# Optimization experiments

Measured on AMD Instinct MI355X. Metric: run time of the kernel, lower is better.

The kernel has to match this reference:

```python
import jax, jax.numpy as jnp
import numpy as np

D_MODEL = 1024
D_STATE = 512
SEQ_LEN = 16384
R_MIN, R_MAX, MAX_PHASE = 0.0, 1.0, 6.28


def setup_inputs() -> dict:
    key = jax.random.key(0)
    ks = jax.random.split(key, 8)
    inputs = jax.random.normal(ks[0], (SEQ_LEN, D_MODEL), dtype=jnp.float32)
    # parameter init exactly as in the module
    u_nu = jax.random.uniform(ks[1], (D_STATE,), dtype=jnp.float32)
    nu_log = jnp.log(-0.5 * jnp.log(u_nu * (R_MAX ** 2 - R_MIN ** 2) + R_MIN ** 2))
    u_th = jax.random.uniform(ks[2], (D_STATE,), dtype=jnp.float32)
    theta_log = jnp.log(MAX_PHASE * u_th)
    diag_lambda = jnp.exp(-jnp.exp(nu_log) + 1j * jnp.exp(theta_log))
    gamma_log = jnp.log(jnp.sqrt(1.0 - jnp.abs(diag_lambda) ** 2))
    bn = jnp.sqrt(jnp.asarray(2 * D_MODEL, jnp.float32))
    cn = jnp.sqrt(jnp.asarray(D_STATE, jnp.float32))
    B_re = jax.random.normal(ks[3], (D_STATE, D_MODEL), dtype=jnp.float32) / bn
    B_im = jax.random.normal(ks[4], (D_STATE, D_MODEL), dtype=jnp.float32) / bn
    C_re = jax.random.normal(ks[5], (D_MODEL, D_STATE), dtype=jnp.float32) / cn
    C_im = jax.random.normal(ks[6], (D_MODEL, D_STATE), dtype=jnp.float32) / cn
    D = jax.random.normal(ks[7], (D_MODEL,), dtype=jnp.float32)
    return {"inputs": inputs, "nu_log": nu_log, "theta_log": theta_log,
            "gamma_log": gamma_log, "B_re": B_re, "B_im": B_im,
            "C_re": C_re, "C_im": C_im, "D": D}


def _binop(q_i, q_j):
    # associative combine for diagonal linear recurrence h' = a*h + b
    a_i, b_i = q_i
    a_j, b_j = q_j
    return (a_j * a_i, a_j * b_i + b_j)


def reference(inputs, nu_log, theta_log, gamma_log, B_re, B_im, C_re, C_im, D):
    L = inputs.shape[0]
    diag_lambda = jnp.exp(-jnp.exp(nu_log) + 1j * jnp.exp(theta_log))  # (d_state,)
    B_norm = (B_re + 1j * B_im) * jnp.exp(gamma_log)[:, None]          # (d_state, d_model)
    C = C_re + 1j * C_im                                               # (d_model, d_state)
    # Bu[t] = B_norm @ x_t  -> (L, d_state) complex
    Bu = inputs.astype(B_norm.dtype) @ B_norm.T
    Lambda_elems = jnp.broadcast_to(diag_lambda, (L, diag_lambda.shape[0]))
    _, h = jax.lax.associative_scan(_binop, (Lambda_elems, Bu))        # (L, d_state)
    # y_t = Re[C h_t] + D * x_t
    return jnp.real(h @ C.T) + D * inputs
```

## Files before the change

### kernel.cpp

```cpp
#include <hip/hip_runtime.h>
#include <math.h>

#define L_SEQ   16384
#define DMODEL  1024
#define NST     512
#define CHUNK   128
#define NCHUNK  (L_SEQ / CHUNK)

typedef float  f32x4 __attribute__((ext_vector_type(4)));
typedef short  s16x8 __attribute__((ext_vector_type(8)));

__device__ __forceinline__ unsigned short f2bf(float f) {
    union { float f; unsigned int u; } v; v.f = f;
    unsigned int r = v.u + 0x7fffu + ((v.u >> 16) & 1u);
    return (unsigned short)(r >> 16);
}
__device__ __forceinline__ unsigned short f2bf_fast(float f) {
    union { float f; unsigned int u; } v; v.f = f;
    return (unsigned short)((v.u + 0x8000u) >> 16);
}
__device__ __forceinline__ float bf2f(unsigned int h16) {
    union { unsigned int u; float f; } v; v.u = h16 << 16; return v.f;
}
__device__ __forceinline__ void mfma16(f32x4& d, s16x8 a, s16x8 b) {
    asm volatile("v_mfma_f32_16x16x32_bf16 %0, %1, %2, %0"
                 : "+v"(d) : "v"(a), "v"(b));
}
__device__ __forceinline__ uint4 pack8(float4 x, float4 y) {
    union { unsigned short u[8]; uint4 v; } t;
    t.u[0] = f2bf_fast(x.x); t.u[1] = f2bf_fast(x.y);
    t.u[2] = f2bf_fast(x.z); t.u[3] = f2bf_fast(x.w);
    t.u[4] = f2bf_fast(y.x); t.u[5] = f2bf_fast(y.y);
    t.u[6] = f2bf_fast(y.z); t.u[7] = f2bf_fast(y.w);
    return t.v;
}

__global__ void setup_params(const float* __restrict__ nu_log,
                             const float* __restrict__ theta_log,
                             float* __restrict__ lam,
                             float* __restrict__ lamH,
                             float* __restrict__ lamT) {
    int s = threadIdx.x;
    if (s >= NST) return;
    float mod = expf(-expf(nu_log[s]));
    float th  = expf(theta_log[s]);
    float ar = mod * cosf(th);
    float ai = mod * sinf(th);
    lam[s] = ar; lam[NST + s] = ai;
    float pr = 1.f, pi = 0.f;
    for (int i = 0; i < CHUNK; ++i) {
        float nr = pr * ar - pi * ai;
        float ni = pr * ai + pi * ar;
        pr = nr; pi = ni;
        if (i == 63) { lamH[s] = pr; lamH[NST + s] = pi; }
    }
    lamT[s] = pr; lamT[NST + s] = pi;
}

__global__ void pack_w1(const float* __restrict__ Bre, const float* __restrict__ Bim,
                        const float* __restrict__ gamma_log, unsigned short* __restrict__ W1) {
    int idx = blockIdx.x * 256 + threadIdx.x;
    int n = idx >> 10, k = idx & 1023;
    int s = n >> 1;
    float g = expf(gamma_log[s]);
    float v = (n & 1) ? Bim[s * DMODEL + k] : Bre[s * DMODEL + k];
    W1[idx] = f2bf(v * g);
}
__global__ void pack_w2(const float* __restrict__ Cre, const float* __restrict__ Cim,
                        unsigned short* __restrict__ W2) {
    int idx = blockIdx.x * 256 + threadIdx.x;
    int n = idx >> 10, k = idx & 1023;
    int s = k >> 1;
    float v = (k & 1) ? -Cim[n * NST + s] : Cre[n * NST + s];
    W2[idx] = f2bf(v);
}

__global__ __launch_bounds__(256)
void gemm1_scan(const float* __restrict__ X, const unsigned short* __restrict__ W1,
                const float* __restrict__ lam,
                unsigned int* __restrict__ Bu, float* __restrict__ ends) {
    const int K = 1024;
    __shared__ __align__(16) unsigned short As[128 * 32];
    __shared__ __align__(16) unsigned short Bs[128 * 32];
    __shared__ __align__(16) unsigned short Ts[128 * 132];

    const int tid  = threadIdx.x;
    const int lane = tid & 63;
    const int wave = tid >> 6;
    const int wr   = wave >> 1, wc = wave & 1;

    const int lin   = blockIdx.y * gridDim.x + blockIdx.x;
    const int n_new = (lin & 7) * 128 + (lin >> 3);
    const int bx = n_new & 7, by = n_new >> 3;
    const int m0 = by * 128, n0 = bx * 128;

    const int srow = tid >> 2;
    const int skb  = (tid & 3) * 8;

    const float*          Ag0 = X  + (size_t)(m0 + srow) * K + skb;
    const float*          Ag1 = Ag0 + (size_t)64 * K;
    const unsigned short* Bg0 = W1 + (size_t)(n0 + srow) * K + skb;
    const unsigned short* Bg1 = Bg0 + (size_t)64 * K;

    f32x4 acc[4][4] = {};

    float4 a00 = *(const float4*)(Ag0);
    float4 a01 = *(const float4*)(Ag0 + 4);
    float4 a10 = *(const float4*)(Ag1);
    float4 a11 = *(const float4*)(Ag1 + 4);
    uint4  rb0 = *(const uint4*)(Bg0);
    uint4  rb1 = *(const uint4*)(Bg1);

    const int fr = lane & 15;
    const int fk = (lane >> 4) * 8;

    for (int k0 = 0; k0 < K; k0 += 32) {
        __syncthreads();
        *(uint4*)&As[srow * 32 + skb]        = pack8(a00, a01);
        *(uint4*)&As[(64 + srow) * 32 + skb] = pack8(a10, a11);
        *(uint4*)&Bs[srow * 32 + skb]        = rb0;
        *(uint4*)&Bs[(64 + srow) * 32 + skb] = rb1;
        __syncthreads();
        if (k0 + 32 < K) {
            a00 = *(const float4*)(Ag0 + k0 + 32);
            a01 = *(const float4*)(Ag0 + k0 + 36);
            a10 = *(const float4*)(Ag1 + k0 + 32);
            a11 = *(const float4*)(Ag1 + k0 + 36);
            rb0 = *(const uint4*)(Bg0 + k0 + 32);
            rb1 = *(const uint4*)(Bg1 + k0 + 32);
        }
        s16x8 af[4], bfq[4];
        #pragma unroll
        for (int i = 0; i < 4; ++i)
            af[i] = *(const s16x8*)&As[(wr * 64 + i * 16 + fr) * 32 + fk];
        #pragma unroll
        for (int j = 0; j < 4; ++j)
            bfq[j] = *(const s16x8*)&Bs[(wc * 64 + j * 16 + fr) * 32 + fk];
        #pragma unroll
        for (int i = 0; i < 4; ++i)
            #pragma unroll
            for (int j = 0; j < 4; ++j)
                mfma16(acc[i][j], af[i], bfq[j]);
    }

    const int crow = (lane >> 4) * 4;
    const int ccol = lane & 15;
    #pragma unroll
    for (int i = 0; i < 4; ++i)
        #pragma unroll
        for (int j = 0; j < 4; ++j)
            #pragma unroll
            for (int r = 0; r < 4; ++r)
                Ts[(wr * 64 + i * 16 + crow + r) * 132 + wc * 64 + j * 16 + ccol]
                    = f2bf_fast(acc[i][j][r]);
    __syncthreads();

    if (tid < 64) {
        const int s  = (n0 >> 1) + tid;
        const float lr = lam[s], li = lam[NST + s];
        float hr = 0.f, hi = 0.f;
        size_t gb = (size_t)m0 * NST + s;
        for (int t = 0; t < 128; ++t) {
            unsigned int v = *(const unsigned int*)&Ts[t * 132 + 2 * tid];
            float br = bf2f(v & 0xffffu), bi = bf2f(v >> 16);
            float nr = fmaf(lr, hr, fmaf(-li, hi, br));
            float ni = fmaf(lr, hi, fmaf( li, hr, bi));
            hr = nr; hi = ni;
            Bu[gb + (size_t)t * NST] =
                (unsigned int)f2bf_fast(hr) | ((unsigned int)f2bf_fast(hi) << 16);
        }
        ends[(size_t)(by * NST + s) * 2]     = hr;
        ends[(size_t)(by * NST + s) * 2 + 1] = hi;
    }
}

__global__ __launch_bounds__(NST)
void scan_carry(const float* __restrict__ ends, const float* __restrict__ lamT,
                float* __restrict__ car) {
    const int s = threadIdx.x;
    const float ar = lamT[s], ai = lamT[NST + s];
    float cr = 0.f, ci = 0.f;
    for (int c = 0; c < NCHUNK; ++c) {
        car[(size_t)(c * NST + s) * 2]     = cr;
        car[(size_t)(c * NST + s) * 2 + 1] = ci;
        float er = ends[(size_t)(c * NST + s) * 2];
        float ei = ends[(size_t)(c * NST + s) * 2 + 1];
        float nr = fmaf(ar, cr, fmaf(-ai, ci, er));
        float ni = fmaf(ar, ci, fmaf( ai, cr, ei));
        cr = nr; ci = ni;
    }
}

__global__ __launch_bounds__(NST)
void scan_apply(unsigned int* __restrict__ Bu, const float* __restrict__ lam,
                const float* __restrict__ lamH, const float* __restrict__ car) {
    const int c    = blockIdx.x >> 1;
    const int half = blockIdx.x & 1;
    if (c == 0) return;
    const int s = threadIdx.x;
    const float lr = lam[s], li = lam[NST + s];
    float pr = car[(size_t)(c * NST + s) * 2];
    float pi = car[(size_t)(c * NST + s) * 2 + 1];
    if (half) {
        float hr = lamH[s], hi = lamH[NST + s];
        float nr = pr * hr - pi * hi;
        float ni = pr * hi + pi * hr;
        pr = nr; pi = ni;
    }
    size_t base = ((size_t)c * CHUNK + half * 64) * NST + s;
    #pragma unroll 4
    for (int t = 0; t < 64; ++t) {
        float nr = lr * pr - li * pi;
        float ni = lr * pi + li * pr;
        pr = nr; pi = ni;
        unsigned int v = Bu[base + (size_t)t * NST];
        float hr = bf2f(v & 0xffffu) + pr;
        float hi = bf2f(v >> 16)     + pi;
        Bu[base + (size_t)t * NST] =
            (unsigned int)f2bf_fast(hr) | ((unsigned int)f2bf_fast(hi) << 16);
    }
}

__global__ __launch_bounds__(256)
void gemm2(const unsigned short* __restrict__ H, const unsigned short* __restrict__ W2,
           float* __restrict__ Y, const float* __restrict__ Dv,
           const float* __restrict__ Xf) {
    const int K = 1024, N = 1024;
    __shared__ __align__(16) unsigned short As[128 * 32];
    __shared__ __align__(16) unsigned short Bs[128 * 32];

    const int tid  = threadIdx.x;
    const int lane = tid & 63;
    const int wave = tid >> 6;
    const int wr   = wave >> 1, wc = wave & 1;

    const int lin   = blockIdx.y * gridDim.x + blockIdx.x;
    const int n_new = (lin & 7) * 128 + (lin >> 3);
    const int bx = n_new & 7, by = n_new >> 3;
    const int m0 = by * 128, n0 = bx * 128;

    const int srow = tid >> 2;
    const int skb  = (tid & 3) * 8;

    const unsigned short* Ag0 = H  + (size_t)(m0 + srow) * K + skb;
    const unsigned short* Ag1 = Ag0 + (size_t)64 * K;
    const unsigned short* Bg0 = W2 + (size_t)(n0 + srow) * K + skb;
    const unsigned short* Bg1 = Bg0 + (size_t)64 * K;

    f32x4 acc[4][4] = {};

    uint4 ra0 = *(const uint4*)Ag0;
    uint4 ra1 = *(const uint4*)Ag1;
    uint4 rb0 = *(const uint4*)Bg0;
    uint4 rb1 = *(const uint4*)Bg1;

    const int fr = lane & 15;
    const int fk = (lane >> 4) * 8;

    for (int k0 = 0; k0 < K; k0 += 32) {
        __syncthreads();
        *(uint4*)&As[srow * 32 + skb]        = ra0;
        *(uint4*)&As[(64 + srow) * 32 + skb] = ra1;
        *(uint4*)&Bs[srow * 32 + skb]        = rb0;
        *(uint4*)&Bs[(64 + srow) * 32 + skb] = rb1;
        __syncthreads();
        if (k0 + 32 < K) {
            ra0 = *(const uint4*)(Ag0 + k0 + 32);
            ra1 = *(const uint4*)(Ag1 + k0 + 32);
            rb0 = *(const uint4*)(Bg0 + k0 + 32);
            rb1 = *(const uint4*)(Bg1 + k0 + 32);
        }
        s16x8 af[4], bfq[4];
        #pragma unroll
        for (int i = 0; i < 4; ++i)
            af[i] = *(const s16x8*)&As[(wr * 64 + i * 16 + fr) * 32 + fk];
        #pragma unroll
        for (int j = 0; j < 4; ++j)
            bfq[j] = *(const s16x8*)&Bs[(wc * 64 + j * 16 + fr) * 32 + fk];
        #pragma unroll
        for (int i = 0; i < 4; ++i)
            #pragma unroll
            for (int j = 0; j < 4; ++j)
                mfma16(acc[i][j], af[i], bfq[j]);
    }

    const int crow = (lane >> 4) * 4;
    const int ccol = lane & 15;
    #pragma unroll
    for (int i = 0; i < 4; ++i) {
        #pragma unroll
        for (int j = 0; j < 4; ++j) {
            const int mbase = m0 + wr * 64 + i * 16 + crow;
            const int n     = n0 + wc * 64 + j * 16 + ccol;
            #pragma unroll
            for (int r = 0; r < 4; ++r) {
                const int m = mbase + r;
                Y[(size_t)m * N + n] = acc[i][j][r] + Dv[n] * Xf[(size_t)m * N + n];
            }
        }
    }
}

extern "C" void kernel_launch(void* const* d_in, const int* in_sizes, int n_in,
                              void* d_out, int out_size, void* d_ws, size_t ws_size,
                              hipStream_t stream) {
    const float* X         = (const float*)d_in[0];
    const float* nu_log    = (const float*)d_in[1];
    const float* theta_log = (const float*)d_in[2];
    const float* gamma_log = (const float*)d_in[3];
    const float* Bre       = (const float*)d_in[4];
    const float* Bim       = (const float*)d_in[5];
    const float* Cre       = (const float*)d_in[6];
    const float* Cim       = (const float*)d_in[7];
    const float* Dv        = (const float*)d_in[8];
    float* Y = (float*)d_out;

    char* ws = (char*)d_ws;
    size_t off = 0;
    unsigned int*   Bu  = (unsigned int*)(ws + off);   off += (size_t)L_SEQ * NST * 4;
    unsigned short* W1  = (unsigned short*)(ws + off); off += (size_t)DMODEL * DMODEL * 2;
    unsigned short* W2  = (unsigned short*)(ws + off); off += (size_t)DMODEL * DMODEL * 2;
    float* lam  = (float*)(ws + off); off += 1024 * 4;
    float* lamH = (float*)(ws + off); off += 1024 * 4;
    float* lamT = (float*)(ws + off); off += 1024 * 4;
    float* ends = (float*)(ws + off); off += (size_t)NCHUNK * NST * 2 * 4;
    float* car  = (float*)(ws + off); off += (size_t)NCHUNK * NST * 2 * 4;

    setup_params<<<1, NST, 0, stream>>>(nu_log, theta_log, lam, lamH, lamT);
    pack_w1<<<(DMODEL * DMODEL) / 256, 256, 0, stream>>>(Bre, Bim, gamma_log, W1);
    pack_w2<<<(DMODEL * DMODEL) / 256, 256, 0, stream>>>(Cre, Cim, W2);

    dim3 gg(8, 128);
    gemm1_scan<<<gg, 256, 0, stream>>>(X, W1, lam, Bu, ends);
    scan_carry<<<1, NST, 0, stream>>>(ends, lamT, car);
    scan_apply<<<2 * NCHUNK, NST, 0, stream>>>(Bu, lam, lamH, car);
    gemm2<<<gg, 256, 0, stream>>>((const unsigned short*)Bu, W2, Y, Dv, X);
}
```

Baseline: 156.4 us.

## Split fused GEMM+chunk scan into separate GEMM, chunk-end scan and full rescan

The chunk-local scan that ran inside the GEMM1 epilogue (only 64 threads active, with an LDS transpose tile) is removed. GEMM1 now writes raw bf16 Bu directly, and a separate scan_ends kernel computes the chunk end states. scan_h then redoes the full recurrence from the carries instead of adding decayed carries. The gamma scaling moves from the packed weights into the scan, and rounding switches to round-to-nearest-even. This frees the GEMM from its serial epilogue at the cost of an extra full read pass over Bu and two extra launches.

```diff
diff --git a/kernel.cpp b/kernel.cpp
--- a/kernel.cpp
+++ b/kernel.cpp
@@ -37,9 +37,10 @@
 
 __global__ void setup_params(const float* __restrict__ nu_log,
                              const float* __restrict__ theta_log,
+                             const float* __restrict__ gamma_log,
                              float* __restrict__ lam,
-                             float* __restrict__ lamH,
-                             float* __restrict__ lamT) {
+                             float* __restrict__ lamT,
+                             float* __restrict__ gam) {
     int s = threadIdx.x;
     if (s >= NST) return;
     float mod = expf(-expf(nu_log[s]));
@@ -47,24 +48,23 @@
     float ar = mod * cosf(th);
     float ai = mod * sinf(th);
     lam[s] = ar; lam[NST + s] = ai;
+    gam[s] = expf(gamma_log[s]);
     float pr = 1.f, pi = 0.f;
     for (int i = 0; i < CHUNK; ++i) {
         float nr = pr * ar - pi * ai;
         float ni = pr * ai + pi * ar;
         pr = nr; pi = ni;
-        if (i == 63) { lamH[s] = pr; lamH[NST + s] = pi; }
     }
     lamT[s] = pr; lamT[NST + s] = pi;
 }
 
 __global__ void pack_w1(const float* __restrict__ Bre, const float* __restrict__ Bim,
-                        const float* __restrict__ gamma_log, unsigned short* __restrict__ W1) {
+                        unsigned short* __restrict__ W1) {
     int idx = blockIdx.x * 256 + threadIdx.x;
     int n = idx >> 10, k = idx & 1023;
     int s = n >> 1;
-    float g = expf(gamma_log[s]);
     float v = (n & 1) ? Bim[s * DMODEL + k] : Bre[s * DMODEL + k];
-    W1[idx] = f2bf(v * g);
+    W1[idx] = f2bf(v);
 }
 __global__ void pack_w2(const float* __restrict__ Cre, const float* __restrict__ Cim,
                         unsigned short* __restrict__ W2) {
@@ -76,13 +76,11 @@
 }
 
 __global__ __launch_bounds__(256)
-void gemm1_scan(const float* __restrict__ X, const unsigned short* __restrict__ W1,
-                const float* __restrict__ lam,
-                unsigned int* __restrict__ Bu, float* __restrict__ ends) {
+void gemm1(const float* __restrict__ X, const unsigned short* __restrict__ W1,
+           unsigned short* __restrict__ Bu) {
     const int K = 1024;
     __shared__ __align__(16) unsigned short As[128 * 32];
     __shared__ __align__(16) unsigned short Bs[128 * 32];
-    __shared__ __align__(16) unsigned short Ts[128 * 132];
 
     const int tid  = threadIdx.x;
     const int lane = tid & 63;
@@ -148,30 +146,34 @@
     #pragma unroll
     for (int i = 0; i < 4; ++i)
         #pragma unroll
-        for (int j = 0; j < 4; ++j)
+        for (int j = 0; j < 4; ++j) {
+            const int mbase = m0 + wr * 64 + i * 16 + crow;
+            const int n     = n0 + wc * 64 + j * 16 + ccol;
             #pragma unroll
             for (int r = 0; r < 4; ++r)
-                Ts[(wr * 64 + i * 16 + crow + r) * 132 + wc * 64 + j * 16 + ccol]
-                    = f2bf_fast(acc[i][j][r]);
-    __syncthreads();
-
-    if (tid < 64) {
-        const int s  = (n0 >> 1) + tid;
-        const float lr = lam[s], li = lam[NST + s];
-        float hr = 0.f, hi = 0.f;
-        size_t gb = (size_t)m0 * NST + s;
-        for (int t = 0; t < 128; ++t) {
-            unsigned int v = *(const unsigned int*)&Ts[t * 132 + 2 * tid];
-            float br = bf2f(v & 0xffffu), bi = bf2f(v >> 16);
-            float nr = fmaf(lr, hr, fmaf(-li, hi, br));
-            float ni = fmaf(lr, hi, fmaf( li, hr, bi));
-            hr = nr; hi = ni;
-            Bu[gb + (size_t)t * NST] =
-                (unsigned int)f2bf_fast(hr) | ((unsigned int)f2bf_fast(hi) << 16);
+                Bu[(size_t)(mbase + r) * 1024 + n] = f2bf(acc[i][j][r]);
         }
-        ends[(size_t)(by * NST + s) * 2]     = hr;
-        ends[(size_t)(by * NST + s) * 2 + 1] = hi;
-    }
+}
+
+__global__ __launch_bounds__(128)
+void scan_ends(const unsigned int* __restrict__ Bu, const float* __restrict__ lam,
+               const float* __restrict__ gam, float* __restrict__ ends) {
+    const int s = blockIdx.y * 128 + threadIdx.x;
+    const int c = blockIdx.x;
+    const float lr = lam[s], li = lam[NST + s], g = gam[s];
+    float hr = 0.f, hi = 0.f;
+    size_t base = (size_t)c * CHUNK * NST + s;
+    #pragma unroll 4
+    for (int t = 0; t < CHUNK; ++t) {
+        unsigned int v = Bu[base + (size_t)t * NST];
+        float br = g * bf2f(v & 0xffffu);
+        float bi = g * bf2f(v >> 16);
+        float nr = fmaf(lr, hr, fmaf(-li, hi, br));
+        float ni = fmaf(lr, hi, fmaf( li, hr, bi));
+        hr = nr; hi = ni;
+    }
+    ends[(size_t)(c * NST + s) * 2]     = hr;
+    ends[(size_t)(c * NST + s) * 2 + 1] = hi;
 }
 
 __global__ __launch_bounds__(NST)
@@ -191,33 +193,25 @@
     }
 }
 
-__global__ __launch_bounds__(NST)
-void scan_apply(unsigned int* __restrict__ Bu, const float* __restrict__ lam,
-                const float* __restrict__ lamH, const float* __restrict__ car) {
-    const int c    = blockIdx.x >> 1;
-    const int half = blockIdx.x & 1;
-    if (c == 0) return;
-    const int s = threadIdx.x;
-    const float lr = lam[s], li = lam[NST + s];
-    float pr = car[(size_t)(c * NST + s) * 2];
-    float pi = car[(size_t)(c * NST + s) * 2 + 1];
-    if (half) {
-        float hr = lamH[s], hi = lamH[NST + s];
-        float nr = pr * hr - pi * hi;
-        float ni = pr * hi + pi * hr;
-        pr = nr; pi = ni;
-    }
-    size_t base = ((size_t)c * CHUNK + half * 64) * NST + s;
+__global__ __launch_bounds__(128)
+void scan_h(unsigned int* __restrict__ Bu, const float* __restrict__ lam,
+            const float* __restrict__ gam, const float* __restrict__ car) {
+    const int s = blockIdx.y * 128 + threadIdx.x;
+    const int c = blockIdx.x;
+    const float lr = lam[s], li = lam[NST + s], g = gam[s];
+    float hr = car[(size_t)(c * NST + s) * 2];
+    float hi = car[(size_t)(c * NST + s) * 2 + 1];
+    size_t base = (size_t)c * CHUNK * NST + s;
     #pragma unroll 4
-    for (int t = 0; t < 64; ++t) {
-        float nr = lr * pr - li * pi;
-        float ni = lr * pi + li * pr;
-        pr = nr; pi = ni;
+    for (int t = 0; t < CHUNK; ++t) {
         unsigned int v = Bu[base + (size_t)t * NST];
-        float hr = bf2f(v & 0xffffu) + pr;
-        float hi = bf2f(v >> 16)     + pi;
+        float br = g * bf2f(v & 0xffffu);
+        float bi = g * bf2f(v >> 16);
+        float nr = fmaf(lr, hr, fmaf(-li, hi, br));
+        float ni = fmaf(lr, hi, fmaf( li, hr, bi));
+        hr = nr; hi = ni;
         Bu[base + (size_t)t * NST] =
-            (unsigned int)f2bf_fast(hr) | ((unsigned int)f2bf_fast(hi) << 16);
+            (unsigned int)f2bf(hr) | ((unsigned int)f2bf(hi) << 16);
     }
 }
 
@@ -317,22 +311,26 @@
 
     char* ws = (char*)d_ws;
     size_t off = 0;
-    unsigned int*   Bu  = (unsigned int*)(ws + off);   off += (size_t)L_SEQ * NST * 4;
+    unsigned short* Bu  = (unsigned short*)(ws + off); off += (size_t)L_SEQ * 1024 * 2;
     unsigned short* W1  = (unsigned short*)(ws + off); off += (size_t)DMODEL * DMODEL * 2;
     unsigned short* W2  = (unsigned short*)(ws + off); off += (size_t)DMODEL * DMODEL * 2;
     float* lam  = (float*)(ws + off); off += 1024 * 4;
-    float* lamH = (float*)(ws + off); off += 1024 * 4;
     float* lamT = (float*)(ws + off); off += 1024 * 4;
+    float* gam  = (float*)(ws + off); off += 512 * 4;
     float* ends = (float*)(ws + off); off += (size_t)NCHUNK * NST * 2 * 4;
     float* car  = (float*)(ws + off); off += (size_t)NCHUNK * NST * 2 * 4;
 
-    setup_params<<<1, NST, 0, stream>>>(nu_log, theta_log, lam, lamH, lamT);
-    pack_w1<<<(DMODEL * DMODEL) / 256, 256, 0, stream>>>(Bre, Bim, gamma_log, W1);
+    setup_params<<<1, NST, 0, stream>>>(nu_log, theta_log, gamma_log, lam, lamT, gam);
+    pack_w1<<<(DMODEL * DMODEL) / 256, 256, 0, stream>>>(Bre, Bim, W1);
     pack_w2<<<(DMODEL * DMODEL) / 256, 256, 0, stream>>>(Cre, Cim, W2);
 
     dim3 gg(8, 128);
-    gemm1_scan<<<gg, 256, 0, stream>>>(X, W1, lam, Bu, ends);
+    gemm1<<<gg, 256, 0, stream>>>(X, W1, Bu);
+
+    dim3 gs(NCHUNK, 4);
+    scan_ends<<<gs, 128, 0, stream>>>((const unsigned int*)Bu, lam, gam, ends);
     scan_carry<<<1, NST, 0, stream>>>(ends, lamT, car);
-    scan_apply<<<2 * NCHUNK, NST, 0, stream>>>(Bu, lam, lamH, car);
-    gemm2<<<gg, 256, 0, stream>>>((const unsigned short*)Bu, W2, Y, Dv, X);
-}
+    scan_h<<<gs, 128, 0, stream>>>((unsigned int*)Bu, lam, gam, car);
+
+    gemm2<<<gg, 256, 0, stream>>>(Bu, W2, Y, Dv, X);
+}
```

After: 168.0 us. 1.07x slower.
